# Optimization experiments

Measured on AMD Instinct MI355X. Metric: run time of the kernel, lower is better.

Reference implementation:

```python
import jax, jax.numpy as jnp
import numpy as np

# Longformer-base-4096 config (layers reduced 12->4 for CPU tractability)
B_, S_, DM, H_, DH, L_, FF, V = 1, 4096, 768, 12, 64, 4, 3072, 50265
BLOCK = 256  # one-sided window; total attention window = 512


def layer_norm(x, g, b, eps=1e-5):
    m = jnp.mean(x, axis=-1, keepdims=True)
    v = jnp.mean(jnp.square(x - m), axis=-1, keepdims=True)
    return (x - m) * jax.lax.rsqrt(v + eps) * g + b


def sliding_attention(q, k, v, key_mask):
    """Banded local attention: each query attends keys within +/- BLOCK positions.
    q,k,v: (B,H,S,Dh); key_mask: (B,S) 1 for valid tokens."""
    B, H, S, D = q.shape
    nb = S // BLOCK
    qb = q.reshape(B, H, nb, BLOCK, D)
    kp = jnp.pad(k, ((0, 0), (0, 0), (BLOCK, BLOCK), (0, 0)))
    vp = jnp.pad(v, ((0, 0), (0, 0), (BLOCK, BLOCK), (0, 0)))
    # each query block n sees key blocks n-1, n, n+1  -> window of 3*BLOCK keys
    idx = jnp.arange(nb)[:, None] * BLOCK + jnp.arange(3 * BLOCK)[None, :]  # (nb, 3B)
    kw = kp[:, :, idx]  # (B,H,nb,3B,D)
    vw = vp[:, :, idx]
    scores = jnp.einsum('bhnqd,bhnkd->bhnqk', qb, kw) / np.float32(np.sqrt(D))
    # relative position of key w.r.t. query inside the 3-block window
    rel = jnp.arange(3 * BLOCK)[None, :] - BLOCK - jnp.arange(BLOCK)[:, None]  # (BLOCK,3B)
    band = (jnp.abs(rel) <= BLOCK)[None, None, None]  # (1,1,1,BLOCK,3B)
    mp = jnp.pad(key_mask.astype(bool), ((0, 0), (BLOCK, BLOCK)))
    mw = mp[:, idx][:, None, :, None, :]  # (B,1,nb,1,3B)
    scores = jnp.where(band & mw, scores, -1e9)
    probs = jax.nn.softmax(scores, axis=-1)
    out = jnp.einsum('bhnqk,bhnkd->bhnqd', probs, vw)
    return out.reshape(B, H, S, D)


def encode(ids, mask, word_emb, pos_emb, emb_g, emb_b, layers):
    B, S = ids.shape
    x = word_emb[ids] + pos_emb[None, :S]
    x = layer_norm(x, emb_g, emb_b)

    def step(x, p):
        wq, bq, wk, bk, wv, bv, wo, bo, g1, b1, w1, c1, w2, c2, g2, b2 = p
        heads = lambda y: y.reshape(B, S, H_, DH).transpose(0, 2, 1, 3)
        q = heads(x @ wq + bq)
        k = heads(x @ wk + bk)
        vv = heads(x @ wv + bv)
        a = sliding_attention(q, k, vv, mask)
        a = a.transpose(0, 2, 1, 3).reshape(B, S, DM) @ wo + bo
        x2 = layer_norm(x + a, g1, b1)  # post-LN (RoBERTa/Longformer)
        h = jax.nn.gelu(x2 @ w1 + c1)
        x3 = layer_norm(x2 + h @ w2 + c2, g2, b2)
        return x3, None

    x, _ = jax.lax.scan(jax.checkpoint(step), x, layers)
    return x


def setup_inputs() -> dict:
    key = jax.random.key(0)
    ks = jax.random.split(key, 16)
    s = 0.02
    d = {
        'input_ids1': jax.random.randint(ks[0], (B_, S_), 0, V),
        'input_ids2': jax.random.randint(ks[1], (B_, S_), 0, V),
        'attention_mask1': jnp.ones((B_, S_), dtype=jnp.int32),
        'attention_mask2': jnp.ones((B_, S_), dtype=jnp.int32),
        'word_emb': jax.random.normal(ks[2], (V, DM)) * s,
        'pos_emb': jax.random.normal(ks[3], (S_, DM)) * s,
        'emb_g': jnp.ones((DM,)), 'emb_b': jnp.zeros((DM,)),
        'wq': jax.random.normal(ks[4], (L_, DM, DM)) * s, 'bq': jnp.zeros((L_, DM)),
        'wk': jax.random.normal(ks[5], (L_, DM, DM)) * s, 'bk': jnp.zeros((L_, DM)),
        'wv': jax.random.normal(ks[6], (L_, DM, DM)) * s, 'bv': jnp.zeros((L_, DM)),
        'wo': jax.random.normal(ks[7], (L_, DM, DM)) * s, 'bo': jnp.zeros((L_, DM)),
        'ln1_g': jnp.ones((L_, DM)), 'ln1_b': jnp.zeros((L_, DM)),
        'w_ff1': jax.random.normal(ks[8], (L_, DM, FF)) * s, 'b_ff1': jnp.zeros((L_, FF)),
        'w_ff2': jax.random.normal(ks[9], (L_, FF, DM)) * s, 'b_ff2': jnp.zeros((L_, DM)),
        'ln2_g': jnp.ones((L_, DM)), 'ln2_b': jnp.zeros((L_, DM)),
        'dense_w': jax.random.normal(ks[10], (DM, 1)) * s, 'dense_b': jnp.zeros((1,)),
    }
    return d


def reference(input_ids1, input_ids2, attention_mask1, attention_mask2,
              word_emb, pos_emb, emb_g, emb_b,
              wq, bq, wk, bk, wv, bv, wo, bo,
              ln1_g, ln1_b, w_ff1, b_ff1, w_ff2, b_ff2, ln2_g, ln2_b,
              dense_w, dense_b):
    layers = (wq, bq, wk, bk, wv, bv, wo, bo, ln1_g, ln1_b,
              w_ff1, b_ff1, w_ff2, b_ff2, ln2_g, ln2_b)
    o1 = encode(input_ids1, attention_mask1, word_emb, pos_emb, emb_g, emb_b, layers)
    o2 = encode(input_ids2, attention_mask2, word_emb, pos_emb, emb_g, emb_b, layers)
    diff = o1.mean(1, keepdims=True) - o2.mean(1, keepdims=True)  # (B,1,DM)
    return jax.nn.sigmoid(diff @ dense_w + dense_b)  # (B,1,1)
```

## Files before the change

kernel.cpp:

```cpp
#include <hip/hip_runtime.h>

typedef __bf16 bf16_t;
typedef bf16_t bf16x8 __attribute__((ext_vector_type(8)));
typedef float f32x4 __attribute__((ext_vector_type(4)));
typedef unsigned short u16x4 __attribute__((ext_vector_type(4)));
typedef unsigned short u16x8 __attribute__((ext_vector_type(8)));
typedef float f32x4v __attribute__((ext_vector_type(4)));

#define NL 4

__device__ __forceinline__ float bf2f(unsigned short u){
  unsigned int x = ((unsigned int)u) << 16;
  return __builtin_bit_cast(float, x);
}
__device__ __forceinline__ unsigned short f2bf(float f){
  unsigned int u = __builtin_bit_cast(unsigned int, f);
  u += 0x7FFFu + ((u >> 16) & 1u);
  return (unsigned short)(u >> 16);
}
__device__ __forceinline__ void gload16(const void* g, void* l){
  __builtin_amdgcn_global_load_lds((const __attribute__((address_space(1))) unsigned int*)g,
                                   (__attribute__((address_space(3))) unsigned int*)l, 16, 0, 0);
}

__global__ __launch_bounds__(256) void transpose_cvt(const float* __restrict__ src,
                                                     unsigned short* __restrict__ dst,
                                                     int R, int C){
  __shared__ unsigned short tile[64][72];
  size_t boff = (size_t)blockIdx.z * (size_t)R * (size_t)C;
  int tc0 = blockIdx.x * 64, tr0 = blockIdx.y * 64;
  int t = threadIdx.x;
  int r = t >> 2, cs = (t & 3) * 16;
  const float* s = src + boff + (size_t)(tr0 + r) * C + tc0 + cs;
  #pragma unroll
  for (int j = 0; j < 16; j += 4){
    f32x4v v = *(const f32x4v*)(s + j);
    #pragma unroll
    for (int q = 0; q < 4; q++) tile[r][cs + j + q] = f2bf(v[q]);
  }
  __syncthreads();
  int n = t >> 2;
  unsigned short* d = dst + boff + (size_t)(tc0 + n) * R + tr0 + cs;
  u16x8 o0, o1;
  #pragma unroll
  for (int j = 0; j < 8; j++){ o0[j] = tile[cs + j][n]; o1[j] = tile[cs + 8 + j][n]; }
  *(u16x8*)d       = o0;
  *(u16x8*)(d + 8) = o1;
}

__global__ __launch_bounds__(256) void transpose64(const unsigned short* __restrict__ src,
                                                   unsigned short* __restrict__ dst,
                                                   int R, int C){
  __shared__ unsigned short tile[64][72];
  size_t boff = (size_t)blockIdx.z * (size_t)R * (size_t)C;
  int tc0 = blockIdx.x * 64, tr0 = blockIdx.y * 64;
  int t = threadIdx.x;
  int r = t >> 2, cs = (t & 3) * 16;
  const unsigned short* s = src + boff + (size_t)(tr0 + r) * C + tc0 + cs;
  *(u16x8*)(&tile[r][cs])     = *(const u16x8*)(s);
  *(u16x8*)(&tile[r][cs + 8]) = *(const u16x8*)(s + 8);
  __syncthreads();
  int n = t >> 2;
  unsigned short* d = dst + boff + (size_t)(tc0 + n) * R + tr0 + cs;
  u16x8 o0, o1;
  #pragma unroll
  for (int j = 0; j < 8; j++){ o0[j] = tile[cs + j][n]; o1[j] = tile[cs + 8 + j][n]; }
  *(u16x8*)d       = o0;
  *(u16x8*)(d + 8) = o1;
}

template<int ACT>
__device__ __forceinline__ void gemm_core(const unsigned short* __restrict__ A,
                                          const unsigned short* __restrict__ BT,
                                          const float* __restrict__ bias,
                                          unsigned short* __restrict__ C,
                                          int m0, int n0, int N, int K){
  __shared__ unsigned short lds[32768];
  const int t = threadIdx.x;
  const int lane = t & 63;
  const int l15 = lane & 15, l4 = lane >> 4;
  const int w = t >> 6, wm = w >> 1, wn = w & 1;
  f32x4 acc[4][4] = {};
  const int rr = t >> 3;
  const int c8 = ((t & 7) ^ (rr & 7)) * 8;
  const unsigned short* Abase = A  + (size_t)(m0 + rr) * K + c8;
  const unsigned short* Bbase = BT + (size_t)(n0 + rr) * K + c8;

  auto STAGE = [&](int k0, int buf){
    unsigned short* As_ = lds + buf * 16384;
    unsigned short* Bs_ = As_ + 8192;
    #pragma unroll
    for (int it = 0; it < 4; it++){
      gload16(Abase + (size_t)(it * 32) * K + k0, As_ + (it * 256 + t) * 8);
      gload16(Bbase + (size_t)(it * 32) * K + k0, Bs_ + (it * 256 + t) * 8);
    }
  };
  auto COMPUTE = [&](int buf){
    const unsigned short* Ab = lds + buf * 16384;
    const unsigned short* Bb = Ab + 8192;
    #pragma unroll
    for (int kk = 0; kk < 2; kk++){
      bf16x8 af[4], bfr[4];
      const int cs = kk * 4;
      #pragma unroll
      for (int i = 0; i < 4; i++){
        const int ra = wm * 64 + i * 16 + l15;
        const int rb = wn * 64 + i * 16 + l15;
        const int so = ((cs + l4) ^ (l15 & 7)) * 8;
        af[i]  = *(const bf16x8*)(Ab + ra * 64 + so);
        bfr[i] = *(const bf16x8*)(Bb + rb * 64 + so);
      }
      #pragma unroll
      for (int j = 0; j < 4; j++)
        #pragma unroll
        for (int i = 0; i < 4; i++)
          acc[j][i] = __builtin_amdgcn_mfma_f32_16x16x32_bf16(bfr[j], af[i], acc[j][i], 0, 0, 0);
    }
  };

  const int S = K >> 6;
  STAGE(0, 0); STAGE(64, 1);
  int cur = 0;
  for (int k = 0; k < S - 2; k++){
    asm volatile("s_waitcnt vmcnt(8)" ::: "memory");
    __builtin_amdgcn_s_barrier();
    __builtin_amdgcn_sched_barrier(0);
    COMPUTE(cur);
    __builtin_amdgcn_sched_barrier(0);
    __builtin_amdgcn_s_barrier();
    STAGE((k + 2) << 6, cur);
    cur ^= 1;
  }
  asm volatile("s_waitcnt vmcnt(8)" ::: "memory");
  __builtin_amdgcn_s_barrier();
  __builtin_amdgcn_sched_barrier(0);
  COMPUTE(cur);
  cur ^= 1;
  asm volatile("s_waitcnt vmcnt(0)" ::: "memory");
  __builtin_amdgcn_s_barrier();
  __builtin_amdgcn_sched_barrier(0);
  COMPUTE(cur);

  const int mB = m0 + wm * 64;
  const int nB = n0 + wn * 64;
  #pragma unroll
  for (int i = 0; i < 4; i++){
    unsigned short* crow = C + (size_t)(mB + i * 16 + l15) * N + nB;
    #pragma unroll
    for (int j = 0; j < 4; j++){
      const int nn = j * 16 + l4 * 4;
      f32x4v bb = *(const f32x4v*)(bias + nB + nn);
      u16x4 pk;
      #pragma unroll
      for (int r = 0; r < 4; r++){
        float v = acc[j][i][r] + bb[r];
        if (ACT == 1){
          float e = __expf(-1.5957691216057308f * (v + 0.044715f * v * v * v));
          v = __fdividef(v, 1.0f + e);
        }
        pk[r] = f2bf(v);
      }
      *(u16x4*)(crow + nn) = pk;
    }
  }
}

template<int ACT>
__global__ __launch_bounds__(256) void gemm_bt(const unsigned short* __restrict__ A,
                                               const unsigned short* __restrict__ BT,
                                               const float* __restrict__ bias,
                                               unsigned short* __restrict__ C, int N, int K){
  const int b = blockIdx.x;
  const int s = b >> 3;
  const int m = (b & 7) * 8 + (s & 7);
  const int n = s >> 3;
  gemm_core<ACT>(A, BT, bias, C, m * 128, n * 128, N, K);
}

__global__ __launch_bounds__(256) void qkv_gemm(const unsigned short* __restrict__ A,
                                                const unsigned short* __restrict__ wT,
                                                int l,
                                                const float* __restrict__ bq,
                                                const float* __restrict__ bk,
                                                const float* __restrict__ bv,
                                                unsigned short* __restrict__ q,
                                                unsigned short* __restrict__ k,
                                                unsigned short* __restrict__ v){
  const int b = blockIdx.x;
  const int s = b >> 3;
  const int m0 = ((b & 7) * 8 + (s & 7)) * 128;
  const int grp = s >> 3;
  const int sel = grp / 6, col = grp % 6;
  const unsigned short* BT = wT + ((size_t)sel * NL + l) * (size_t)(768 * 768);
  const float* bias = sel == 0 ? bq : (sel == 1 ? bk : bv);
  unsigned short* C = sel == 0 ? q : (sel == 1 ? k : v);
  gemm_core<0>(A, BT, bias, C, m0, col * 128, 768, 768);
}

__global__ __launch_bounds__(256, 4) void attn_kernel(const unsigned short* __restrict__ Q,
                                                      const unsigned short* __restrict__ Km,
                                                      const unsigned short* __restrict__ VT,
                                                      const int* __restrict__ mask1,
                                                      const int* __restrict__ mask2,
                                                      unsigned short* __restrict__ O){
  const int qt = blockIdx.x, h = blockIdx.y, seq = blockIdx.z;
  const int t = threadIdx.x, lane = t & 63, w = t >> 6;
  const int l15 = lane & 15, l4 = lane >> 4;
  __shared__ unsigned short Kc[64 * 64];
  __shared__ unsigned short VTc[64 * 64];
  __shared__ unsigned short Ps[4][16 * 64];
  const unsigned short* Qp  = Q  + (size_t)seq * 4096 * 768;
  const unsigned short* Kp  = Km + (size_t)seq * 4096 * 768;
  const unsigned short* VTp = VT + (size_t)seq * 768 * 4096;
  const int* mask = seq ? mask2 : mask1;
  unsigned short* Op = O + (size_t)seq * 4096 * 768;

  const int q0 = qt * 64 + w * 16;
  const int qg = q0 + l15;
  const int swz = (l15 & 7) * 8;

  bf16x8 qf[2];
  #pragma unroll
  for (int ks = 0; ks < 2; ks++)
    qf[ks] = *(const bf16x8*)(Qp + (size_t)qg * 768 + h * 64 + ks * 32 + l4 * 8);

  f32x4 oacc[4] = {};
  float rm = -1e30f, rl = 0.0f;

  const int kstart = qt * 64 >= 256 ? qt * 64 - 256 : 0;
  const int kend0  = qt * 64 + 320;
  const int kend   = kend0 > 4096 ? 4096 : kend0;
  unsigned short* psw = &Ps[w][0];

  const int rr = t >> 3;
  const int c8 = (((t & 7) ^ (rr & 7)) * 8);

  for (int kb = kstart; kb < kend; kb += 64){
    gload16(Kp  + (size_t)(kb + rr) * 768 + h * 64 + c8,       Kc + t * 8);
    gload16(Kp  + (size_t)(kb + 32 + rr) * 768 + h * 64 + c8,  Kc + 2048 + t * 8);
    gload16(VTp + (size_t)(h * 64 + rr) * 4096 + kb + c8,      VTc + t * 8);
    gload16(VTp + (size_t)(h * 64 + 32 + rr) * 4096 + kb + c8, VTc + 2048 + t * 8);
    __syncthreads();
    if (kb + 63 >= q0 - 256 && kb <= q0 + 271){
      f32x4 sT[4];
      #pragma unroll
      for (int mt = 0; mt < 4; mt++){
        const unsigned short* kr = Kc + (mt * 16 + l15) * 64;
        bf16x8 kf0 = *(const bf16x8*)(kr + ((l4 * 8) ^ swz));
        bf16x8 kf1 = *(const bf16x8*)(kr + ((32 + l4 * 8) ^ swz));
        f32x4 z = {};
        z      = __builtin_amdgcn_mfma_f32_16x16x32_bf16(kf0, qf[0], z, 0, 0, 0);
        sT[mt] = __builtin_amdgcn_mfma_f32_16x16x32_bf16(kf1, qf[1], z, 0, 0, 0);
      }
      float smax = -1e30f;
      #pragma unroll
      for (int mt = 0; mt < 4; mt++){
        int4 mv = *(const int4*)(mask + kb + mt * 16 + l4 * 4);
        #pragma unroll
        for (int r = 0; r < 4; r++){
          int kgl = kb + mt * 16 + l4 * 4 + r;
          int d = kgl - qg;
          int mvv = (r == 0) ? mv.x : (r == 1) ? mv.y : (r == 2) ? mv.z : mv.w;
          bool ok = (mvv != 0) && (d <= 256) && (d >= -256);
          float v = sT[mt][r] * 0.125f;
          sT[mt][r] = ok ? v : -1e30f;
          smax = fmaxf(smax, sT[mt][r]);
        }
      }
      smax = fmaxf(smax, __shfl_xor(smax, 16, 64));
      smax = fmaxf(smax, __shfl_xor(smax, 32, 64));
      float nm = fmaxf(rm, smax);
      float sc = __expf(rm - nm);
      rm = nm;
      float psum = 0.0f;
      #pragma unroll
      for (int mt = 0; mt < 4; mt++){
        u16x4 pk;
        #pragma unroll
        for (int r = 0; r < 4; r++){
          float p = (sT[mt][r] > -1e29f) ? __expf(sT[mt][r] - nm) : 0.0f;
          psum += p;
          pk[r] = f2bf(p);
        }
        *(u16x4*)(psw + l15 * 64 + ((mt * 16 + l4 * 4) ^ swz)) = pk;
      }
      psum += __shfl_xor(psum, 16, 64);
      psum += __shfl_xor(psum, 32, 64);
      rl = rl * sc + psum;
      float scq[4];
      #pragma unroll
      for (int r = 0; r < 4; r++) scq[r] = __shfl(sc, l4 * 4 + r, 64);
      #pragma unroll
      for (int g = 0; g < 4; g++)
        #pragma unroll
        for (int r = 0; r < 4; r++) oacc[g][r] *= scq[r];
      asm volatile("s_waitcnt lgkmcnt(0)" ::: "memory");
      __builtin_amdgcn_sched_barrier(0);
      bf16x8 pa0 = *(const bf16x8*)(psw + l15 * 64 + ((l4 * 8) ^ swz));
      bf16x8 pa1 = *(const bf16x8*)(psw + l15 * 64 + ((32 + l4 * 8) ^ swz));
      #pragma unroll
      for (int g = 0; g < 4; g++){
        const unsigned short* vr = VTc + (g * 16 + l15) * 64;
        bf16x8 vb0 = *(const bf16x8*)(vr + ((l4 * 8) ^ swz));
        bf16x8 vb1 = *(const bf16x8*)(vr + ((32 + l4 * 8) ^ swz));
        oacc[g] = __builtin_amdgcn_mfma_f32_16x16x32_bf16(pa0, vb0, oacc[g], 0, 0, 0);
        oacc[g] = __builtin_amdgcn_mfma_f32_16x16x32_bf16(pa1, vb1, oacc[g], 0, 0, 0);
      }
    }
    __syncthreads();
  }
  float rlq[4];
  #pragma unroll
  for (int r = 0; r < 4; r++) rlq[r] = __shfl(rl, l4 * 4 + r, 64);
  #pragma unroll
  for (int g = 0; g < 4; g++)
    #pragma unroll
    for (int r = 0; r < 4; r++){
      float v = oacc[g][r] / rlq[r];
      Op[(size_t)(q0 + l4 * 4 + r) * 768 + h * 64 + g * 16 + l15] = f2bf(v);
    }
}

__global__ __launch_bounds__(192) void embed_ln(const int* __restrict__ ids1,
                                                const int* __restrict__ ids2,
                                                const float* __restrict__ we,
                                                const float* __restrict__ pe,
                                                const float* __restrict__ g,
                                                const float* __restrict__ b,
                                                unsigned short* __restrict__ out){
  const int row = blockIdx.x;
  const int seq = row >> 12, s = row & 4095;
  const int t = threadIdx.x;
  const int id = (seq ? ids2 : ids1)[s];
  f32x4v wvv = *(const f32x4v*)(we + (size_t)id * 768 + t * 4);
  f32x4v pv  = *(const f32x4v*)(pe + (size_t)s * 768 + t * 4);
  float v[4];
  #pragma unroll
  for (int j = 0; j < 4; j++) v[j] = wvv[j] + pv[j];
  float sum = 0, ss = 0;
  #pragma unroll
  for (int j = 0; j < 4; j++){ sum += v[j]; ss += v[j] * v[j]; }
  for (int off = 1; off < 64; off <<= 1){ sum += __shfl_xor(sum, off, 64); ss += __shfl_xor(ss, off, 64); }
  __shared__ float red[2][3];
  int wid = t >> 6;
  if ((t & 63) == 0){ red[0][wid] = sum; red[1][wid] = ss; }
  __syncthreads();
  sum = red[0][0] + red[0][1] + red[0][2];
  ss  = red[1][0] + red[1][1] + red[1][2];
  float mean = sum * (1.0f / 768.0f);
  float var  = ss * (1.0f / 768.0f) - mean * mean;
  float rstd = rsqrtf(var + 1e-5f);
  f32x4v gv = *(const f32x4v*)(g + t * 4);
  f32x4v bv = *(const f32x4v*)(b + t * 4);
  u16x4 o;
  #pragma unroll
  for (int j = 0; j < 4; j++) o[j] = f2bf((v[j] - mean) * rstd * gv[j] + bv[j]);
  *(u16x4*)(out + (size_t)row * 768 + t * 4) = o;
}

__global__ __launch_bounds__(192) void add_ln(const unsigned short* __restrict__ A,
                                              const unsigned short* __restrict__ Bp,
                                              const float* __restrict__ g,
                                              const float* __restrict__ b,
                                              unsigned short* __restrict__ out){
  const int row = blockIdx.x;
  const int t = threadIdx.x;
  u16x4 a4 = *(const u16x4*)(A  + (size_t)row * 768 + t * 4);
  u16x4 b4 = *(const u16x4*)(Bp + (size_t)row * 768 + t * 4);
  float v[4];
  #pragma unroll
  for (int j = 0; j < 4; j++) v[j] = bf2f(a4[j]) + bf2f(b4[j]);
  float sum = 0, ss = 0;
  #pragma unroll
  for (int j = 0; j < 4; j++){ sum += v[j]; ss += v[j] * v[j]; }
  for (int off = 1; off < 64; off <<= 1){ sum += __shfl_xor(sum, off, 64); ss += __shfl_xor(ss, off, 64); }
  __shared__ float red[2][3];
  int wid = t >> 6;
  if ((t & 63) == 0){ red[0][wid] = sum; red[1][wid] = ss; }
  __syncthreads();
  sum = red[0][0] + red[0][1] + red[0][2];
  ss  = red[1][0] + red[1][1] + red[1][2];
  float mean = sum * (1.0f / 768.0f);
  float var  = ss * (1.0f / 768.0f) - mean * mean;
  float rstd = rsqrtf(var + 1e-5f);
  f32x4v gv = *(const f32x4v*)(g + t * 4);
  f32x4v bv = *(const f32x4v*)(b + t * 4);
  u16x4 o;
  #pragma unroll
  for (int j = 0; j < 4; j++) o[j] = f2bf((v[j] - mean) * rstd * gv[j] + bv[j]);
  *(u16x4*)(out + (size_t)row * 768 + t * 4) = o;
}

__global__ __launch_bounds__(256) void colmean(const unsigned short* __restrict__ X,
                                               float* __restrict__ mean){
  const int t = threadIdx.x;
  const int seq = blockIdx.y;
  const int r0 = blockIdx.x * 64;
  const unsigned short* base = X + ((size_t)seq * 4096 + r0) * 768;
  float a0 = 0, a1 = 0, a2 = 0;
  for (int r = 0; r < 64; r++){
    const unsigned short* p = base + (size_t)r * 768;
    a0 += bf2f(p[t]);
    a1 += bf2f(p[t + 256]);
    a2 += bf2f(p[t + 512]);
  }
  atomicAdd(&mean[seq * 768 + t], a0);
  atomicAdd(&mean[seq * 768 + t + 256], a1);
  atomicAdd(&mean[seq * 768 + t + 512], a2);
}

__global__ __launch_bounds__(256) void final_k(const float* __restrict__ means,
                                               const float* __restrict__ dw,
                                               const float* __restrict__ db,
                                               float* __restrict__ out){
  const int t = threadIdx.x;
  float part = 0;
  for (int c = t; c < 768; c += 256)
    part += (means[c] - means[768 + c]) * (1.0f / 4096.0f) * dw[c];
  for (int off = 1; off < 64; off <<= 1) part += __shfl_xor(part, off, 64);
  __shared__ float red[4];
  if ((t & 63) == 0) red[t >> 6] = part;
  __syncthreads();
  if (t == 0){
    float r = red[0] + red[1] + red[2] + red[3] + db[0];
    out[0] = 1.0f / (1.0f + expf(-r));
  }
}

__global__ void sentinel_k(float* out){ out[0] = -1.0f; }

extern "C" void kernel_launch(void* const* d_in, const int* in_sizes, int n_in,
                              void* d_out, int out_size, void* d_ws, size_t ws_size,
                              hipStream_t stream){
  (void)in_sizes; (void)n_in; (void)out_size;
  const int* ids1  = (const int*)d_in[0];
  const int* ids2  = (const int*)d_in[1];
  const int* mask1 = (const int*)d_in[2];
  const int* mask2 = (const int*)d_in[3];
  const float* we = (const float*)d_in[4];
  const float* pe = (const float*)d_in[5];
  const float* eg = (const float*)d_in[6];
  const float* eb = (const float*)d_in[7];
  const float* wq = (const float*)d_in[8];
  const float* bq = (const float*)d_in[9];
  const float* wk = (const float*)d_in[10];
  const float* bk = (const float*)d_in[11];
  const float* wv = (const float*)d_in[12];
  const float* bv = (const float*)d_in[13];
  const float* wo = (const float*)d_in[14];
  const float* bo = (const float*)d_in[15];
  const float* g1 = (const float*)d_in[16];
  const float* b1 = (const float*)d_in[17];
  const float* w1 = (const float*)d_in[18];
  const float* c1 = (const float*)d_in[19];
  const float* w2 = (const float*)d_in[20];
  const float* c2 = (const float*)d_in[21];
  const float* g2 = (const float*)d_in[22];
  const float* b2 = (const float*)d_in[23];
  const float* dw = (const float*)d_in[24];
  const float* db = (const float*)d_in[25];
  float* outp = (float*)d_out;

  char* ws = (char*)d_ws;
  size_t off = 0;
  auto alloc = [&](size_t bytes) -> char* {
    char* p = ws + off;
    off += (bytes + 255) & ~(size_t)255;
    return p;
  };
  const size_t W768 = (size_t)768 * 768;
  const size_t WFF  = (size_t)768 * 3072;
  unsigned short* wqkvT = (unsigned short*)alloc(3 * NL * W768 * 2);
  unsigned short* woT   = (unsigned short*)alloc(NL * W768 * 2);
  unsigned short* w1T   = (unsigned short*)alloc(NL * WFF * 2);
  unsigned short* w2T   = (unsigned short*)alloc(NL * WFF * 2);
  unsigned short* xb    = (unsigned short*)alloc((size_t)8192 * 768 * 2);
  unsigned short* qb_   = (unsigned short*)alloc((size_t)8192 * 768 * 2);
  unsigned short* kb_   = (unsigned short*)alloc((size_t)8192 * 768 * 2);
  unsigned short* vb_   = (unsigned short*)alloc((size_t)8192 * 768 * 2);
  unsigned short* hb    = (unsigned short*)alloc((size_t)8192 * 3072 * 2);
  unsigned short* vt    = (unsigned short*)alloc((size_t)2 * 768 * 4096 * 2);
  float* means          = (float*)alloc(2 * 768 * 4);
  if (off > ws_size){ sentinel_k<<<1, 1, 0, stream>>>(outp); return; }

  transpose_cvt<<<dim3(12, 12, NL), 256, 0, stream>>>(wq, wqkvT,                 768, 768);
  transpose_cvt<<<dim3(12, 12, NL), 256, 0, stream>>>(wk, wqkvT + NL * W768,     768, 768);
  transpose_cvt<<<dim3(12, 12, NL), 256, 0, stream>>>(wv, wqkvT + 2 * NL * W768, 768, 768);
  transpose_cvt<<<dim3(12, 12, NL), 256, 0, stream>>>(wo, woT,                   768, 768);
  transpose_cvt<<<dim3(48, 12, NL), 256, 0, stream>>>(w1, w1T,                   768, 3072);
  transpose_cvt<<<dim3(12, 48, NL), 256, 0, stream>>>(w2, w2T,                   3072, 768);

  embed_ln<<<8192, 192, 0, stream>>>(ids1, ids2, we, pe, eg, eb, xb);

  for (int l = 0; l < NL; l++){
    qkv_gemm<<<1152, 256, 0, stream>>>(xb, wqkvT, l, bq + l * 768, bk + l * 768, bv + l * 768,
                                       qb_, kb_, vb_);
    transpose64<<<dim3(12, 64, 2), 256, 0, stream>>>(vb_, vt, 4096, 768);
    attn_kernel<<<dim3(64, 12, 2), 256, 0, stream>>>(qb_, kb_, vt, mask1, mask2, vb_);
    gemm_bt<0><<<384, 256, 0, stream>>>(vb_, woT + (size_t)l * W768, bo + l * 768, qb_, 768, 768);
    add_ln<<<8192, 192, 0, stream>>>(xb, qb_, g1 + l * 768, b1 + l * 768, kb_);
    gemm_bt<1><<<1536, 256, 0, stream>>>(kb_, w1T + (size_t)l * WFF, c1 + l * 3072, hb, 3072, 768);
    gemm_bt<0><<<384, 256, 0, stream>>>(hb, w2T + (size_t)l * WFF, c2 + l * 768, vb_, 768, 3072);
    add_ln<<<8192, 192, 0, stream>>>(kb_, vb_, g2 + l * 768, b2 + l * 768, xb);
  }

  hipMemsetAsync(means, 0, 2 * 768 * 4, stream);
  colmean<<<dim3(64, 2), 256, 0, stream>>>(xb, means);
  final_k<<<1, 256, 0, stream>>>(means, dw, db, outp);
}
```

Before: 1.025 ms.

## Use 256x256-tile double-buffered GEMM kernel for FFN1 projection

Adds a new gemm256 kernel with 512 threads, 256x256 output tiles, swizzled LDS and a two-stage global_load_lds double buffer, then uses it for the FFN up-projection with GELU. Larger tiles raise arithmetic intensity and cut redundant A/B loads compared with the 128-tile gemm_bt. The cost is 128KB of dynamic LDS per block, which limits occupancy to one block per CU, and a grid of only 384 blocks, which may leave CUs unevenly loaded.

```diff
diff --git a/kernel.cpp b/kernel.cpp
--- a/kernel.cpp
+++ b/kernel.cpp
@@ -195,6 +195,108 @@
   const float* bias = sel == 0 ? bq : (sel == 1 ? bk : bv);
   unsigned short* C = sel == 0 ? q : (sel == 1 ? k : v);
   gemm_core<0>(A, BT, bias, C, m0, col * 128, 768, 768);
+}
+
+template<int ACT>
+__global__ __launch_bounds__(512, 2) void gemm256(const unsigned short* __restrict__ A,
+                                                  const unsigned short* __restrict__ BT,
+                                                  const float* __restrict__ bias,
+                                                  unsigned short* __restrict__ C, int N, int K){
+  extern __shared__ unsigned short lds256[];
+  const int b = blockIdx.x;
+  const int s = b >> 3;
+  const int m0 = ((b & 7) * 4 + (s & 3)) * 256;
+  const int n0 = (s >> 2) * 256;
+  const int t = threadIdx.x;
+  const int lane = t & 63;
+  const int l15 = lane & 15, l4 = lane >> 4;
+  const int w = t >> 6;
+  const int wm = w >> 2, wn = w & 3;
+  f32x4 acc[4][8] = {};
+  const int rr = t >> 3;
+  const int c8 = ((t & 7) ^ (rr & 7)) * 8;
+  const unsigned short* Abase = A  + (size_t)(m0 + rr) * K + c8;
+  const unsigned short* Bbase = BT + (size_t)(n0 + rr) * K + c8;
+
+  auto STAGE = [&](int k0, int buf){
+    unsigned short* As_ = lds256 + buf * 32768;
+    unsigned short* Bs_ = As_ + 16384;
+    #pragma unroll
+    for (int it = 0; it < 4; it++){
+      gload16(Abase + (size_t)(it * 64) * K + k0, As_ + (it * 512 + t) * 8);
+      gload16(Bbase + (size_t)(it * 64) * K + k0, Bs_ + (it * 512 + t) * 8);
+    }
+  };
+  auto COMPUTE = [&](int buf){
+    const unsigned short* Ab = lds256 + buf * 32768;
+    const unsigned short* Bb = Ab + 16384;
+    #pragma unroll
+    for (int kk = 0; kk < 2; kk++){
+      bf16x8 af[8], bfr[4];
+      const int cs = kk * 4;
+      #pragma unroll
+      for (int i = 0; i < 8; i++){
+        const int ra = wm * 128 + i * 16 + l15;
+        af[i] = *(const bf16x8*)(Ab + ra * 64 + (((cs + l4) ^ (l15 & 7)) * 8));
+      }
+      #pragma unroll
+      for (int j = 0; j < 4; j++){
+        const int rb = wn * 64 + j * 16 + l15;
+        bfr[j] = *(const bf16x8*)(Bb + rb * 64 + (((cs + l4) ^ (l15 & 7)) * 8));
+      }
+      #pragma unroll
+      for (int j = 0; j < 4; j++)
+        #pragma unroll
+        for (int i = 0; i < 8; i++)
+          acc[j][i] = __builtin_amdgcn_mfma_f32_16x16x32_bf16(bfr[j], af[i], acc[j][i], 0, 0, 0);
+    }
+  };
+
+  const int S = K >> 6;
+  STAGE(0, 0); STAGE(64, 1);
+  int cur = 0;
+  for (int k = 0; k < S - 2; k++){
+    asm volatile("s_waitcnt vmcnt(8)" ::: "memory");
+    __builtin_amdgcn_s_barrier();
+    __builtin_amdgcn_sched_barrier(0);
+    COMPUTE(cur);
+    __builtin_amdgcn_sched_barrier(0);
+    __builtin_amdgcn_s_barrier();
+    STAGE((k + 2) << 6, cur);
+    cur ^= 1;
+  }
+  asm volatile("s_waitcnt vmcnt(8)" ::: "memory");
+  __builtin_amdgcn_s_barrier();
+  __builtin_amdgcn_sched_barrier(0);
+  COMPUTE(cur);
+  cur ^= 1;
+  asm volatile("s_waitcnt vmcnt(0)" ::: "memory");
+  __builtin_amdgcn_s_barrier();
+  __builtin_amdgcn_sched_barrier(0);
+  COMPUTE(cur);
+
+  const int mB = m0 + wm * 128;
+  const int nB = n0 + wn * 64;
+  #pragma unroll
+  for (int i = 0; i < 8; i++){
+    unsigned short* crow = C + (size_t)(mB + i * 16 + l15) * N + nB;
+    #pragma unroll
+    for (int j = 0; j < 4; j++){
+      const int nn = j * 16 + l4 * 4;
+      f32x4v bb = *(const f32x4v*)(bias + nB + nn);
+      u16x4 pk;
+      #pragma unroll
+      for (int r = 0; r < 4; r++){
+        float v = acc[j][i][r] + bb[r];
+        if (ACT == 1){
+          float e = __expf(-1.5957691216057308f * (v + 0.044715f * v * v * v));
+          v = __fdividef(v, 1.0f + e);
+        }
+        pk[r] = f2bf(v);
+      }
+      *(u16x4*)(crow + nn) = pk;
+    }
+  }
 }
 
 __global__ __launch_bounds__(256, 4) void attn_kernel(const unsigned short* __restrict__ Q,
@@ -499,7 +601,7 @@
     attn_kernel<<<dim3(64, 12, 2), 256, 0, stream>>>(qb_, kb_, vt, mask1, mask2, vb_);
     gemm_bt<0><<<384, 256, 0, stream>>>(vb_, woT + (size_t)l * W768, bo + l * 768, qb_, 768, 768);
     add_ln<<<8192, 192, 0, stream>>>(xb, qb_, g1 + l * 768, b1 + l * 768, kb_);
-    gemm_bt<1><<<1536, 256, 0, stream>>>(kb_, w1T + (size_t)l * WFF, c1 + l * 3072, hb, 3072, 768);
+    gemm256<1><<<384, 512, 131072, stream>>>(kb_, w1T + (size_t)l * WFF, c1 + l * 3072, hb, 3072, 768);
     gemm_bt<0><<<384, 256, 0, stream>>>(hb, w2T + (size_t)l * WFF, c2 + l * 768, vb_, 768, 3072);
     add_ln<<<8192, 192, 0, stream>>>(kb_, vb_, g2 + l * 768, b2 + l * 768, xb);
   }
```

After: 1.077 ms. +5.1%, slower.

## Fuse V transpose into QKV GEMM epilogue, merge weight transposes, add setprio

Applied to the files above, without the earlier changes.

The QKV GEMM now writes V directly in transposed (head-dim-major) layout through a new store mode, which removes the separate transpose64 kernel launched once per layer. The four 768x768 weight transpose-convert launches are merged into one launch, and s_setprio raises wave priority around the MFMA compute phases. The transposed V store is a scattered 2-byte write with a 4096-element stride, so the qkv_gemm epilogue for V blocks may get more expensive in exchange for dropping a full read-write pass.

```diff
diff --git a/kernel.cpp b/kernel.cpp
--- a/kernel.cpp
+++ b/kernel.cpp
@@ -21,6 +21,37 @@
 __device__ __forceinline__ void gload16(const void* g, void* l){
   __builtin_amdgcn_global_load_lds((const __attribute__((address_space(1))) unsigned int*)g,
                                    (__attribute__((address_space(3))) unsigned int*)l, 16, 0, 0);
+}
+
+__global__ __launch_bounds__(256) void transpose_cvt16(const float* __restrict__ wq,
+                                                       const float* __restrict__ wk,
+                                                       const float* __restrict__ wv,
+                                                       const float* __restrict__ wo,
+                                                       unsigned short* __restrict__ wqkvT,
+                                                       unsigned short* __restrict__ woT){
+  __shared__ unsigned short tile[64][72];
+  const int zi = blockIdx.z;
+  const size_t W = (size_t)768 * 768;
+  const float* src = (zi < 4 ? wq : zi < 8 ? wk : zi < 12 ? wv : wo) + (size_t)(zi & 3) * W;
+  unsigned short* dst = (zi < 12 ? wqkvT + (size_t)zi * W : woT + (size_t)(zi - 12) * W);
+  int tc0 = blockIdx.x * 64, tr0 = blockIdx.y * 64;
+  int t = threadIdx.x;
+  int r = t >> 2, cs = (t & 3) * 16;
+  const float* s = src + (size_t)(tr0 + r) * 768 + tc0 + cs;
+  #pragma unroll
+  for (int j = 0; j < 16; j += 4){
+    f32x4v v = *(const f32x4v*)(s + j);
+    #pragma unroll
+    for (int q = 0; q < 4; q++) tile[r][cs + j + q] = f2bf(v[q]);
+  }
+  __syncthreads();
+  int n = t >> 2;
+  unsigned short* d = dst + (size_t)(tc0 + n) * 768 + tr0 + cs;
+  u16x8 o0, o1;
+  #pragma unroll
+  for (int j = 0; j < 8; j++){ o0[j] = tile[cs + j][n]; o1[j] = tile[cs + 8 + j][n]; }
+  *(u16x8*)d       = o0;
+  *(u16x8*)(d + 8) = o1;
 }
 
 __global__ __launch_bounds__(256) void transpose_cvt(const float* __restrict__ src,
@@ -48,28 +79,7 @@
   *(u16x8*)(d + 8) = o1;
 }
 
-__global__ __launch_bounds__(256) void transpose64(const unsigned short* __restrict__ src,
-                                                   unsigned short* __restrict__ dst,
-                                                   int R, int C){
-  __shared__ unsigned short tile[64][72];
-  size_t boff = (size_t)blockIdx.z * (size_t)R * (size_t)C;
-  int tc0 = blockIdx.x * 64, tr0 = blockIdx.y * 64;
-  int t = threadIdx.x;
-  int r = t >> 2, cs = (t & 3) * 16;
-  const unsigned short* s = src + boff + (size_t)(tr0 + r) * C + tc0 + cs;
-  *(u16x8*)(&tile[r][cs])     = *(const u16x8*)(s);
-  *(u16x8*)(&tile[r][cs + 8]) = *(const u16x8*)(s + 8);
-  __syncthreads();
-  int n = t >> 2;
-  unsigned short* d = dst + boff + (size_t)(tc0 + n) * R + tr0 + cs;
-  u16x8 o0, o1;
-  #pragma unroll
-  for (int j = 0; j < 8; j++){ o0[j] = tile[cs + j][n]; o1[j] = tile[cs + 8 + j][n]; }
-  *(u16x8*)d       = o0;
-  *(u16x8*)(d + 8) = o1;
-}
-
-template<int ACT>
+template<int ACT, int STORE_MODE>
 __device__ __forceinline__ void gemm_core(const unsigned short* __restrict__ A,
                                           const unsigned short* __restrict__ BT,
                                           const float* __restrict__ bias,
@@ -125,7 +135,9 @@
     asm volatile("s_waitcnt vmcnt(8)" ::: "memory");
     __builtin_amdgcn_s_barrier();
     __builtin_amdgcn_sched_barrier(0);
+    __builtin_amdgcn_s_setprio(1);
     COMPUTE(cur);
+    __builtin_amdgcn_s_setprio(0);
     __builtin_amdgcn_sched_barrier(0);
     __builtin_amdgcn_s_barrier();
     STAGE((k + 2) << 6, cur);
@@ -134,33 +146,53 @@
   asm volatile("s_waitcnt vmcnt(8)" ::: "memory");
   __builtin_amdgcn_s_barrier();
   __builtin_amdgcn_sched_barrier(0);
+  __builtin_amdgcn_s_setprio(1);
   COMPUTE(cur);
+  __builtin_amdgcn_s_setprio(0);
   cur ^= 1;
   asm volatile("s_waitcnt vmcnt(0)" ::: "memory");
   __builtin_amdgcn_s_barrier();
   __builtin_amdgcn_sched_barrier(0);
+  __builtin_amdgcn_s_setprio(1);
   COMPUTE(cur);
+  __builtin_amdgcn_s_setprio(0);
 
   const int mB = m0 + wm * 64;
   const int nB = n0 + wn * 64;
-  #pragma unroll
-  for (int i = 0; i < 4; i++){
-    unsigned short* crow = C + (size_t)(mB + i * 16 + l15) * N + nB;
-    #pragma unroll
-    for (int j = 0; j < 4; j++){
-      const int nn = j * 16 + l4 * 4;
-      f32x4v bb = *(const f32x4v*)(bias + nB + nn);
-      u16x4 pk;
-      #pragma unroll
-      for (int r = 0; r < 4; r++){
-        float v = acc[j][i][r] + bb[r];
-        if (ACT == 1){
-          float e = __expf(-1.5957691216057308f * (v + 0.044715f * v * v * v));
-          v = __fdividef(v, 1.0f + e);
+  if (STORE_MODE == 0){
+    #pragma unroll
+    for (int i = 0; i < 4; i++){
+      unsigned short* crow = C + (size_t)(mB + i * 16 + l15) * N + nB;
+      #pragma unroll
+      for (int j = 0; j < 4; j++){
+        const int nn = j * 16 + l4 * 4;
+        f32x4v bb = *(const f32x4v*)(bias + nB + nn);
+        u16x4 pk;
+        #pragma unroll
+        for (int r = 0; r < 4; r++){
+          float v = acc[j][i][r] + bb[r];
+          if (ACT == 1){
+            float e = __expf(-1.5957691216057308f * (v + 0.044715f * v * v * v));
+            v = __fdividef(v, 1.0f + e);
+          }
+          pk[r] = f2bf(v);
         }
-        pk[r] = f2bf(v);
-      }
-      *(u16x4*)(crow + nn) = pk;
+        *(u16x4*)(crow + nn) = pk;
+      }
+    }
+  } else {
+    #pragma unroll
+    for (int i = 0; i < 4; i++){
+      const int m = mB + i * 16 + l15;
+      unsigned short* vbase = C + (size_t)(m >> 12) * 768 * 4096 + (m & 4095);
+      #pragma unroll
+      for (int j = 0; j < 4; j++){
+        const int nn = nB + j * 16 + l4 * 4;
+        f32x4v bb = *(const f32x4v*)(bias + nn);
+        #pragma unroll
+        for (int r = 0; r < 4; r++)
+          vbase[(size_t)(nn + r) * 4096] = f2bf(acc[j][i][r] + bb[r]);
+      }
     }
   }
 }
@@ -174,7 +206,7 @@
   const int s = b >> 3;
   const int m = (b & 7) * 8 + (s & 7);
   const int n = s >> 3;
-  gemm_core<ACT>(A, BT, bias, C, m * 128, n * 128, N, K);
+  gemm_core<ACT, 0>(A, BT, bias, C, m * 128, n * 128, N, K);
 }
 
 __global__ __launch_bounds__(256) void qkv_gemm(const unsigned short* __restrict__ A,
@@ -185,16 +217,16 @@
                                                 const float* __restrict__ bv,
                                                 unsigned short* __restrict__ q,
                                                 unsigned short* __restrict__ k,
-                                                unsigned short* __restrict__ v){
+                                                unsigned short* __restrict__ vt){
   const int b = blockIdx.x;
   const int s = b >> 3;
   const int m0 = ((b & 7) * 8 + (s & 7)) * 128;
   const int grp = s >> 3;
   const int sel = grp / 6, col = grp % 6;
   const unsigned short* BT = wT + ((size_t)sel * NL + l) * (size_t)(768 * 768);
-  const float* bias = sel == 0 ? bq : (sel == 1 ? bk : bv);
-  unsigned short* C = sel == 0 ? q : (sel == 1 ? k : v);
-  gemm_core<0>(A, BT, bias, C, m0, col * 128, 768, 768);
+  if (sel == 0)      gemm_core<0, 0>(A, BT, bq, q,  m0, col * 128, 768, 768);
+  else if (sel == 1) gemm_core<0, 0>(A, BT, bk, k,  m0, col * 128, 768, 768);
+  else               gemm_core<0, 2>(A, BT, bv, vt, m0, col * 128, 768, 768);
 }
 
 __global__ __launch_bounds__(256, 4) void attn_kernel(const unsigned short* __restrict__ Q,
@@ -483,19 +515,15 @@
   float* means          = (float*)alloc(2 * 768 * 4);
   if (off > ws_size){ sentinel_k<<<1, 1, 0, stream>>>(outp); return; }
 
-  transpose_cvt<<<dim3(12, 12, NL), 256, 0, stream>>>(wq, wqkvT,                 768, 768);
-  transpose_cvt<<<dim3(12, 12, NL), 256, 0, stream>>>(wk, wqkvT + NL * W768,     768, 768);
-  transpose_cvt<<<dim3(12, 12, NL), 256, 0, stream>>>(wv, wqkvT + 2 * NL * W768, 768, 768);
-  transpose_cvt<<<dim3(12, 12, NL), 256, 0, stream>>>(wo, woT,                   768, 768);
-  transpose_cvt<<<dim3(48, 12, NL), 256, 0, stream>>>(w1, w1T,                   768, 3072);
-  transpose_cvt<<<dim3(12, 48, NL), 256, 0, stream>>>(w2, w2T,                   3072, 768);
+  transpose_cvt16<<<dim3(12, 12, 16), 256, 0, stream>>>(wq, wk, wv, wo, wqkvT, woT);
+  transpose_cvt<<<dim3(48, 12, NL), 256, 0, stream>>>(w1, w1T, 768, 3072);
+  transpose_cvt<<<dim3(12, 48, NL), 256, 0, stream>>>(w2, w2T, 3072, 768);
 
   embed_ln<<<8192, 192, 0, stream>>>(ids1, ids2, we, pe, eg, eb, xb);
 
   for (int l = 0; l < NL; l++){
     qkv_gemm<<<1152, 256, 0, stream>>>(xb, wqkvT, l, bq + l * 768, bk + l * 768, bv + l * 768,
-                                       qb_, kb_, vb_);
-    transpose64<<<dim3(12, 64, 2), 256, 0, stream>>>(vb_, vt, 4096, 768);
+                                       qb_, kb_, vt);
     attn_kernel<<<dim3(64, 12, 2), 256, 0, stream>>>(qb_, kb_, vt, mask1, mask2, vb_);
     gemm_bt<0><<<384, 256, 0, stream>>>(vb_, woT + (size_t)l * W768, bo + l * 768, qb_, 768, 768);
     add_ln<<<8192, 192, 0, stream>>>(xb, qb_, g1 + l * 768, b1 + l * 768, kb_);
```

Result: slower. 1.080 ms (+5.4%).
